# Kernel tuning notes

Measured on AMD Instinct MI355X. Metric: run time of the kernel, lower is better.

## Reference

```python
import jax, jax.numpy as jnp
import numpy as np

# hyperparameters (from init_kwargs)
A_LOG = 1.0
B_LOG = 1.0
C_LOG = 1.0
THR = 0.5
DT = 1.0
EPS = 1e-5


@jax.custom_vjp
def spike(v_scaled):
    # Heaviside forward, fast-sigmoid surrogate backward
    return (v_scaled > 0).astype(jnp.float32)

def _spike_fwd(v_scaled):
    return spike(v_scaled), v_scaled

def _spike_bwd(v_scaled, dy):
    return (dy / (1.0 + 100.0 * jnp.abs(v_scaled)) ** 2,)

spike.defvjp(_spike_fwd, _spike_bwd)


def setup_inputs() -> dict:
    key = jax.random.key(0)
    k1, k2, k3 = jax.random.split(key, 3)
    T, B, N_IN, N_REC = 1000, 128, 256, 256
    x = jax.random.normal(k1, (T, B, N_IN), dtype=jnp.float32)
    z0 = jnp.zeros((B, N_REC), dtype=jnp.float32)
    v0 = jnp.zeros((B, N_REC), dtype=jnp.float32)
    t0 = jnp.zeros((B, N_REC), dtype=jnp.float32)
    # RandomNormal(stddev=0.01) init for input weights
    w_in = 0.01 * jax.random.normal(k2, (N_IN, N_REC), dtype=jnp.float32)
    # recurrence enabled: small random recurrent weights
    w_rec = 0.01 * jax.random.normal(k3, (N_REC, N_REC), dtype=jnp.float32)
    return {"x": x, "z0": z0, "v0": v0, "t0": t0, "w_in": w_in, "w_rec": w_rec}


def _step(carry, x_t, w_in, w_rec):
    z, v, t = carry                              # each [B, n_rec]
    i_in = x_t @ w_in + z @ w_rec                # [B, n_rec]
    h = (i_in != 0).astype(jnp.float32)          # activity flag
    new_t = t + (1.0 - h)                        # (h != 1) == 1 - h since h in {0,1}
    new_v = v * (1.0 - z)                        # reset on spike
    low_pass = (new_v > -1.0).astype(jnp.float32)
    new_v = new_v - (1.0 - low_pass) * (new_v + 1.0)   # clamp at -1
    # logarithmic leak
    cap = (jnp.exp2(jnp.abs(new_v) / C_LOG) - B_LOG) / A_LOG
    arg = jnp.minimum(DT * h * (new_t + 1.0), cap)
    new_v = new_v - jnp.sign(new_v) * C_LOG * jnp.log2(EPS + A_LOG * arg + B_LOG)
    new_v = new_v + i_in
    new_t = new_t * (1.0 - h)
    new_z = spike((new_v - THR) / THR)
    return (new_z, new_v, new_t), (new_z, new_v)


def reference(x, z0, v0, t0, w_in, w_rec):
    def step(carry, x_t):
        return _step(carry, x_t, w_in, w_rec)
    _, (zs, vs) = jax.lax.scan(step, (z0, v0, t0), x)
    return zs, vs  # each [T, B, n_rec]
```

## Files before the change

kernel.cpp:

```cpp
#include <hip/hip_runtime.h>

__global__ __launch_bounds__(256) void gemm_xw(const float* __restrict__ X,
                                               const float* __restrict__ W,
                                               float* __restrict__ Y,
                                               int M) {
    __shared__ float As[32][132];
    __shared__ float Bs[32][128];

    const int tid = threadIdx.x;
    const int mb = blockIdx.x >> 1;
    const int nb = blockIdx.x & 1;
    const int m0 = mb << 7;
    const int n0 = nb << 7;
    const int tr = (tid >> 4) << 3;
    const int tc = (tid & 15) << 3;

    float acc[8][8];
#pragma unroll
    for (int i = 0; i < 8; ++i)
#pragma unroll
        for (int j = 0; j < 8; ++j) acc[i][j] = 0.f;

    for (int kb = 0; kb < 256; kb += 32) {
#pragma unroll
        for (int i = 0; i < 4; ++i) {
            int f = tid + (i << 8);
            int row = f >> 3, kq = f & 7;
            float4 a = *(const float4*)(X + (size_t)(m0 + row) * 256 + kb + (kq << 2));
            As[(kq << 2) + 0][row] = a.x;
            As[(kq << 2) + 1][row] = a.y;
            As[(kq << 2) + 2][row] = a.z;
            As[(kq << 2) + 3][row] = a.w;
            int rowb = f >> 5, cq = f & 31;
            *(float4*)&Bs[rowb][cq << 2] =
                *(const float4*)(W + (size_t)(kb + rowb) * 256 + n0 + (cq << 2));
        }
        __syncthreads();
#pragma unroll
        for (int k = 0; k < 32; ++k) {
            float a[8], b[8];
            *(float4*)&a[0] = *(const float4*)&As[k][tr];
            *(float4*)&a[4] = *(const float4*)&As[k][tr + 4];
            *(float4*)&b[0] = *(const float4*)&Bs[k][tc];
            *(float4*)&b[4] = *(const float4*)&Bs[k][tc + 4];
#pragma unroll
            for (int i = 0; i < 8; ++i)
#pragma unroll
                for (int j = 0; j < 8; ++j)
                    acc[i][j] = fmaf(a[i], b[j], acc[i][j]);
        }
        __syncthreads();
    }
#pragma unroll
    for (int i = 0; i < 8; ++i) {
        float* yp = Y + (size_t)(m0 + tr + i) * 256 + n0 + tc;
        *(float4*)yp = make_float4(acc[i][0], acc[i][1], acc[i][2], acc[i][3]);
        *(float4*)(yp + 4) = make_float4(acc[i][4], acc[i][5], acc[i][6], acc[i][7]);
    }
}

__global__ __launch_bounds__(256) void lif_seq(const float* __restrict__ ix,
                                               const float* __restrict__ wrec,
                                               const float* __restrict__ z0,
                                               const float* __restrict__ v0,
                                               const float* __restrict__ t0,
                                               float* __restrict__ zs,
                                               float* __restrict__ vs,
                                               int T, int B) {
    const int b = blockIdx.x;
    const int n = threadIdx.x;
    const int w = n >> 6;
    const size_t sb = (size_t)b * 256 + n;
    const size_t stride = (size_t)B * 256;

    __shared__ unsigned long long smask[2][4];

    float v = v0[sb];
    float t = t0[sb];
    float z = z0[sb];

    {
        unsigned long long m = __ballot(z != 0.f);
        if ((n & 63) == 0) smask[0][w] = m;
    }
    __syncthreads();
    unsigned long long mk0 = smask[0][0];
    unsigned long long mk1 = smask[0][1];
    unsigned long long mk2 = smask[0][2];
    unsigned long long mk3 = smask[0][3];
    int p = 1;

    const float* ixp = ix + sb;

    auto step = [&](int ts, float r) {
        float ir = 0.f;
        unsigned long long mm;
        mm = mk0;
        while (mm) { int j = __builtin_ctzll(mm); mm &= mm - 1;
                     ir += wrec[((size_t)j << 8) + n]; }
        mm = mk1;
        while (mm) { int j = __builtin_ctzll(mm); mm &= mm - 1;
                     ir += wrec[((size_t)(64 + j) << 8) + n]; }
        mm = mk2;
        while (mm) { int j = __builtin_ctzll(mm); mm &= mm - 1;
                     ir += wrec[((size_t)(128 + j) << 8) + n]; }
        mm = mk3;
        while (mm) { int j = __builtin_ctzll(mm); mm &= mm - 1;
                     ir += wrec[((size_t)(192 + j) << 8) + n]; }

        float i_in = r + ir;
        float h = (i_in != 0.f) ? 1.f : 0.f;
        float nt = t + (1.f - h);
        float nv = (z != 0.f) ? 0.f : v;
        nv = fmaxf(nv, -1.f);
        float cap = __builtin_amdgcn_exp2f(fabsf(nv)) - 1.f;
        float arg = fminf(h * (nt + 1.f), cap);
        float L = __builtin_amdgcn_logf((1e-5f + arg) + 1.f);
        float sgn = (nv > 0.f) ? 1.f : ((nv < 0.f) ? -1.f : 0.f);
        nv = fmaf(-sgn, L, nv);
        nv = nv + i_in;
        nt = nt * (1.f - h);
        float nz = ((nv - 0.5f) > 0.f) ? 1.f : 0.f;

        v = nv; t = nt; z = nz;

        unsigned long long mw = __ballot(nz != 0.f);
        if ((n & 63) == 0) smask[p][w] = mw;
        __syncthreads();
        mk0 = smask[p][0];
        mk1 = smask[p][1];
        mk2 = smask[p][2];
        mk3 = smask[p][3];
        p ^= 1;

        size_t o = (size_t)ts * stride + sb;
        zs[o] = nz;
        vs[o] = nv;
    };

    float buf[8];
#pragma unroll
    for (int u = 0; u < 8; ++u) buf[u] = ixp[(size_t)u * stride];

    for (int tb = 0; tb < T; tb += 8) {
#pragma unroll
        for (int u = 0; u < 8; ++u) {
            step(tb + u, buf[u]);
            int tn = tb + u + 8;
            tn = (tn < T) ? tn : (T - 1);
            buf[u] = ixp[(size_t)tn * stride];
        }
    }
}

extern "C" void kernel_launch(void* const* d_in, const int* in_sizes, int n_in,
                              void* d_out, int out_size, void* d_ws, size_t ws_size,
                              hipStream_t stream) {
    const float* x    = (const float*)d_in[0];
    const float* z0   = (const float*)d_in[1];
    const float* v0   = (const float*)d_in[2];
    const float* t0   = (const float*)d_in[3];
    const float* w_in = (const float*)d_in[4];
    const float* wrec = (const float*)d_in[5];

    const int n_rec = 256;
    const int B = in_sizes[1] / n_rec;
    const int nin = in_sizes[4] / n_rec;
    const int T = in_sizes[0] / (B * nin);
    const int M = T * B;

    float* zs = (float*)d_out;
    float* vs = zs + (size_t)T * B * n_rec;
    float* ixbuf = zs;

    gemm_xw<<<dim3((M / 128) * 2), dim3(256), 0, stream>>>(x, w_in, ixbuf, M);
    lif_seq<<<dim3(B), dim3(256), 0, stream>>>(ixbuf, wrec, z0, v0, t0, zs, vs, T, B);
}
```

Baseline: 536.3 us.

## Restructure LIF recurrence to overlap mask sync with speculative no-spike update

Moves the spike ballot and barrier to the start of each step and speculatively computes the neuron update assuming no recurrent input. The sparse recurrent gather and recompute then run only when some neuron spiked. The exp2/log math is simplified to a single log of a min. Input prefetch becomes double-buffered 4-step chunks with batched output stores. The cost is duplicated transcendental work whenever spikes occur, and the output stores are deferred within each chunk.

```diff
diff --git a/kernel.cpp b/kernel.cpp
--- a/kernel.cpp
+++ b/kernel.cpp
@@ -59,97 +59,129 @@
     }
 }
 
-__global__ __launch_bounds__(256) void lif_seq(const float* __restrict__ ix,
-                                               const float* __restrict__ wrec,
-                                               const float* __restrict__ z0,
-                                               const float* __restrict__ v0,
-                                               const float* __restrict__ t0,
-                                               float* __restrict__ zs,
-                                               float* __restrict__ vs,
-                                               int T, int B) {
+__global__ __launch_bounds__(256) void lif_seq4(const float* __restrict__ ix,
+                                                const float* __restrict__ wrec,
+                                                const float* __restrict__ z0,
+                                                const float* __restrict__ v0,
+                                                const float* __restrict__ t0,
+                                                float* __restrict__ zs,
+                                                float* __restrict__ vs,
+                                                int T, int B) {
     const int b = blockIdx.x;
-    const int n = threadIdx.x;
-    const int w = n >> 6;
-    const size_t sb = (size_t)b * 256 + n;
+    const int tid = threadIdx.x;
+    const int wv = tid >> 6;
+    const int lane = tid & 63;
+    const size_t sb = (size_t)b * 256 + tid;
     const size_t stride = (size_t)B * 256;
 
     __shared__ unsigned long long smask[2][4];
 
     float v = v0[sb];
     float t = t0[sb];
-    float z = z0[sb];
-
-    {
-        unsigned long long m = __ballot(z != 0.f);
-        if ((n & 63) == 0) smask[0][w] = m;
-    }
-    __syncthreads();
-    unsigned long long mk0 = smask[0][0];
-    unsigned long long mk1 = smask[0][1];
-    unsigned long long mk2 = smask[0][2];
-    unsigned long long mk3 = smask[0][3];
-    int p = 1;
+    bool sp = (z0[sb] != 0.f);
+    int p = 0;
 
     const float* ixp = ix + sb;
 
-    auto step = [&](int ts, float r) {
-        float ir = 0.f;
-        unsigned long long mm;
-        mm = mk0;
-        while (mm) { int j = __builtin_ctzll(mm); mm &= mm - 1;
-                     ir += wrec[((size_t)j << 8) + n]; }
-        mm = mk1;
-        while (mm) { int j = __builtin_ctzll(mm); mm &= mm - 1;
-                     ir += wrec[((size_t)(64 + j) << 8) + n]; }
-        mm = mk2;
-        while (mm) { int j = __builtin_ctzll(mm); mm &= mm - 1;
-                     ir += wrec[((size_t)(128 + j) << 8) + n]; }
-        mm = mk3;
-        while (mm) { int j = __builtin_ctzll(mm); mm &= mm - 1;
-                     ir += wrec[((size_t)(192 + j) << 8) + n]; }
-
-        float i_in = r + ir;
-        float h = (i_in != 0.f) ? 1.f : 0.f;
-        float nt = t + (1.f - h);
-        float nv = (z != 0.f) ? 0.f : v;
-        nv = fmaxf(nv, -1.f);
-        float cap = __builtin_amdgcn_exp2f(fabsf(nv)) - 1.f;
-        float arg = fminf(h * (nt + 1.f), cap);
-        float L = __builtin_amdgcn_logf((1e-5f + arg) + 1.f);
-        float sgn = (nv > 0.f) ? 1.f : ((nv < 0.f) ? -1.f : 0.f);
-        nv = fmaf(-sgn, L, nv);
-        nv = nv + i_in;
-        nt = nt * (1.f - h);
-        float nz = ((nv - 0.5f) > 0.f) ? 1.f : 0.f;
-
-        v = nv; t = nt; z = nz;
-
-        unsigned long long mw = __ballot(nz != 0.f);
-        if ((n & 63) == 0) smask[p][w] = mw;
+    constexpr float G0 = 1e-5f + 1.0f;
+
+    auto step = [&](float rr, float& zo_, float& vo_) {
+        unsigned long long mk = __ballot(sp);
+        if (lane == 0) smask[p][wv] = mk;
         __syncthreads();
-        mk0 = smask[p][0];
-        mk1 = smask[p][1];
-        mk2 = smask[p][2];
-        mk3 = smask[p][3];
+        unsigned long long m0 = smask[p][0];
+        unsigned long long m1 = smask[p][1];
+        unsigned long long m2 = smask[p][2];
+        unsigned long long m3 = smask[p][3];
         p ^= 1;
 
+        float vc = fmaxf(sp ? 0.f : v, -1.f);
+        float E  = __builtin_amdgcn_exp2f(fabsf(vc));
+        float cA = (1e-5f + (E - 1.f)) + 1.f;
+        float tp1 = t + 1.f;
+        bool hz = (rr == 0.f);
+        float cT = hz ? G0 : ((1e-5f + tp1) + 1.f);
+        float L  = __builtin_amdgcn_logf(fminf(cT, cA));
+        float Ls = copysignf(L, vc);
+        float nvp = (vc == 0.f) ? vc : (vc - Ls);
+        float nv  = nvp + rr;
+        float ntn = hz ? tp1 : 0.f;
+
+        if ((m0 | m1 | m2 | m3) != 0ull) {
+            float ir = 0.f;
+            unsigned long long mm;
+            mm = m0;
+            while (mm) { int j = __builtin_ctzll(mm); mm &= mm - 1;
+                ir += wrec[((size_t)j << 8) + tid]; }
+            mm = m1;
+            while (mm) { int j = __builtin_ctzll(mm); mm &= mm - 1;
+                ir += wrec[((size_t)(64 + j) << 8) + tid]; }
+            mm = m2;
+            while (mm) { int j = __builtin_ctzll(mm); mm &= mm - 1;
+                ir += wrec[((size_t)(128 + j) << 8) + tid]; }
+            mm = m3;
+            while (mm) { int j = __builtin_ctzll(mm); mm &= mm - 1;
+                ir += wrec[((size_t)(192 + j) << 8) + tid]; }
+
+            float i_in = rr + ir;
+            bool hz2 = (i_in == 0.f);
+            float cT2 = hz2 ? G0 : ((1e-5f + tp1) + 1.f);
+            float L2  = __builtin_amdgcn_logf(fminf(cT2, cA));
+            float Ls2 = copysignf(L2, vc);
+            float nvp2 = (vc == 0.f) ? vc : (vc - Ls2);
+            nv  = nvp2 + i_in;
+            ntn = hz2 ? tp1 : 0.f;
+        }
+
+        sp = (nv > 0.5f);
+        v = nv;
+        t = ntn;
+        zo_ = sp ? 1.f : 0.f;
+        vo_ = nv;
+    };
+
+    float iA[4], iB[4], zo[4], vo[4];
+
+    auto loadChunk = [&](float (&bf)[4], int c0) {
+#pragma unroll
+        for (int u = 0; u < 4; ++u) {
+            int r = c0 + u;
+            r = (r < T) ? r : T - 1;
+            bf[u] = ixp[(size_t)r * stride];
+        }
+    };
+
+    auto runChunk = [&](float (&bf)[4], int c0) {
+#pragma unroll
+        for (int u = 0; u < 4; ++u) step(bf[u], zo[u], vo[u]);
+#pragma unroll
+        for (int u = 0; u < 4; ++u) {
+            size_t o = (size_t)(c0 + u) * stride + sb;
+            zs[o] = zo[u];
+            vs[o] = vo[u];
+        }
+    };
+
+    loadChunk(iA, 0);
+    int c = 0;
+    while (c + 8 <= T) {
+        loadChunk(iB, c + 4);
+        runChunk(iA, c);
+        loadChunk(iA, c + 8);
+        runChunk(iB, c + 4);
+        c += 8;
+    }
+    if (c + 4 <= T) {
+        runChunk(iA, c);
+        c += 4;
+    }
+    for (int ts = c; ts < T; ++ts) {
+        float r = ixp[(size_t)ts * stride];
+        float zz, vv;
+        step(r, zz, vv);
         size_t o = (size_t)ts * stride + sb;
-        zs[o] = nz;
-        vs[o] = nv;
-    };
-
-    float buf[8];
-#pragma unroll
-    for (int u = 0; u < 8; ++u) buf[u] = ixp[(size_t)u * stride];
-
-    for (int tb = 0; tb < T; tb += 8) {
-#pragma unroll
-        for (int u = 0; u < 8; ++u) {
-            step(tb + u, buf[u]);
-            int tn = tb + u + 8;
-            tn = (tn < T) ? tn : (T - 1);
-            buf[u] = ixp[(size_t)tn * stride];
-        }
+        zs[o] = zz;
+        vs[o] = vv;
     }
 }
 
@@ -174,5 +206,5 @@
     float* ixbuf = zs;
 
     gemm_xw<<<dim3((M / 128) * 2), dim3(256), 0, stream>>>(x, w_in, ixbuf, M);
-    lif_seq<<<dim3(B), dim3(256), 0, stream>>>(ixbuf, wrec, z0, v0, t0, zs, vs, T, B);
+    lif_seq4<<<dim3(B), dim3(256), 0, stream>>>(ixbuf, wrec, z0, v0, t0, zs, vs, T, B);
 }
```

After: 498.9 us. -7.0%, faster.
